# Kernel tuning notes

Hardware: AMD Instinct MI355X
Metric: run time of the kernel (lower is better)

Reference implementation:

```python
import jax, jax.numpy as jnp
import numpy as np

E4M3_MAX = 448.0
M, K, N = 131072, 512, 512


def _round_to_fp8_e4m3(x):
    # Emulated round-to-nearest E4M3: 3 mantissa bits, exponent in [-7, 8]
    abs_x = jnp.abs(x)
    sign = jnp.sign(x)
    exponent = jnp.clip(jnp.floor(jnp.log2(jnp.maximum(abs_x, 2.0 ** -9))), -7.0, 8.0)
    pow2e = jnp.exp2(exponent)
    mantissa = jnp.round(abs_x / pow2e * 8.0) / 8.0  # jnp.round is half-to-even, matching torch.round
    return sign * mantissa * pow2e


def _quantize_e4m3(x, scale):
    scaled = jnp.clip(x * scale, -E4M3_MAX, E4M3_MAX)
    return _round_to_fp8_e4m3(scaled)


def _dynamic_scale(x):
    # FP8TensorMeta.compute_scale with a single amax in history: max_value / amax * 0.9
    amax = jnp.max(jnp.abs(x))
    return jnp.where(amax > 0, E4M3_MAX / amax * 0.9, 1.0)


def setup_inputs() -> dict:
    key = jax.random.key(0)
    k1, k2, k3 = jax.random.split(key, 3)
    bound = 1.0 / np.sqrt(K)  # kaiming_uniform(a=sqrt(5)) on [N,K] -> U(-1/sqrt(K), 1/sqrt(K))
    x = jax.random.normal(k1, (M, K), dtype=jnp.float32)
    weight = jax.random.uniform(k2, (N, K), dtype=jnp.float32, minval=-bound, maxval=bound)
    bias = jax.random.uniform(k3, (N,), dtype=jnp.float32, minval=-bound, maxval=bound)
    return {"x": x, "weight": weight, "bias": bias}


def reference(x, weight, bias):
    input_scale = _dynamic_scale(x)
    weight_scale = _dynamic_scale(weight)
    x_fp8 = _quantize_e4m3(x, input_scale)          # [M, K]
    w_fp8 = _quantize_e4m3(weight, weight_scale)    # [N, K]
    out = jnp.einsum("mk,nk->mn", x_fp8, w_fp8) + bias  # F.linear
    return out / (input_scale * weight_scale)
```

## Files before the change

kernel.cpp:

```cpp
#include <hip/hip_runtime.h>

typedef unsigned short u16;
typedef unsigned int u32;
typedef unsigned char u8;
typedef __attribute__((ext_vector_type(4))) float f32x4;

template <bool HI>
__device__ __forceinline__ u32 q2fp8(float a, float b, u32 old, float s) {
  a = fminf(448.0f, fmaxf(-448.0f, a * s));
  b = fminf(448.0f, fmaxf(-448.0f, b * s));
  return (u32)__builtin_amdgcn_cvt_pk_fp8_f32(a, b, (int)old, HI);
}

__device__ __forceinline__ float block_max(float m) {
#pragma unroll
  for (int off = 32; off > 0; off >>= 1)
    m = fmaxf(m, __shfl_down(m, off, 64));
  __shared__ float sm[4];
  int wv = threadIdx.x >> 6;
  if ((threadIdx.x & 63) == 0) sm[wv] = m;
  __syncthreads();
  float r = fmaxf(fmaxf(sm[0], sm[1]), fmaxf(sm[2], sm[3]));
  __syncthreads();
  return r;
}

#define XBLOCKS 2048
#define WBLOCKS 64

__global__ void amax2_kernel(const float4* __restrict__ x, int nx4,
                             const float4* __restrict__ w, int nw4,
                             float* __restrict__ px, float* __restrict__ pw) {
  int bid = blockIdx.x;
  const float4* p;
  int n4, b, nb;
  float* dst;
  if (bid < XBLOCKS) { p = x; n4 = nx4; dst = px; b = bid; nb = XBLOCKS; }
  else { p = w; n4 = nw4; dst = pw; b = bid - XBLOCKS; nb = WBLOCKS; }
  float m = 0.0f;
  int stride = nb * 256;
  for (int i = b * 256 + threadIdx.x; i < n4; i += stride) {
    float4 v = p[i];
    m = fmaxf(m, fmaxf(fmaxf(fabsf(v.x), fabsf(v.y)), fmaxf(fabsf(v.z), fabsf(v.w))));
  }
  m = block_max(m);
  if (threadIdx.x == 0) dst[b] = m;
}

__global__ void scales_kernel(const float* __restrict__ px, const float* __restrict__ pw,
                              float* __restrict__ wsf) {
  int tid = threadIdx.x;
  float mx = 0.0f;
  for (int i = tid; i < XBLOCKS; i += 256) mx = fmaxf(mx, px[i]);
  mx = block_max(mx);
  float mw = tid < WBLOCKS ? pw[tid] : 0.0f;
  mw = block_max(mw);
  if (tid == 0) {
    float sx = mx > 0.0f ? 448.0f / mx * 0.9f : 1.0f;
    float sw = mw > 0.0f ? 448.0f / mw * 0.9f : 1.0f;
    wsf[2] = sx;
    wsf[3] = sw;
    wsf[4] = 1.0f / (sx * sw);
  }
}

__global__ void quant_w_kernel(const float* __restrict__ w, u8* __restrict__ wq,
                               const float* __restrict__ wsf) {
  const float sw = wsf[3];
  const int id = blockIdx.x * blockDim.x + threadIdx.x;
  const int kc = id >> 9;
  const int n = id & 511;
  const float4* src = (const float4*)(w + (size_t)n * 512 + kc * 8);
  const float4 a = src[0];
  const float4 b = src[1];
  uint2 r;
  r.x = q2fp8<false>(a.x, a.y, 0u, sw);
  r.x = q2fp8<true>(a.z, a.w, r.x, sw);
  r.y = q2fp8<false>(b.x, b.y, 0u, sw);
  r.y = q2fp8<true>(b.z, b.w, r.y, sw);
  *(uint2*)&wq[(size_t)kc * 4096 + n * 8] = r;
}

__global__ void __launch_bounds__(512, 4) gemm_kernel(const float* __restrict__ x,
                                                      const u8* __restrict__ wq,
                                                      const float* __restrict__ bias,
                                                      float* __restrict__ out,
                                                      const float* __restrict__ wsf) {
  __shared__ __align__(16) u8 As[2 * 8192];
  __shared__ __align__(16) u8 Bs[3 * 16384];
  const int tid = threadIdx.x;
  const int lane = tid & 63;
  const int wv = tid >> 6;
  const int quad = lane >> 4;
  const int lr = lane & 15;

  const int lin = blockIdx.x;
  const int xcd = lin & 7;
  const int jn = (lin >> 3) & 1;
  const int grp = lin >> 4;
  const int m0 = (grp * 8 + xcd) * 128;
  const int n0 = jn * 256;

  const float sx = wsf[2];
  const float inv = wsf[4];
  const int wm = (wv >> 2) * 64;
  const int wn = (wv & 3) * 64;
  const int xrow = tid >> 2;
  const int xq0 = (tid & 3) * 2;

  f32x4 acc[4][4] = {};
  float4 xr[4];

  auto stageB = [&](int bu, int kt) {
#pragma unroll
    for (int i = 0; i < 2; ++i) {
      const u8* gp = wq + (size_t)(kt * 8 + wv) * 4096 + (size_t)n0 * 8 + i * 1024 + lane * 16;
      u8* lp = &Bs[bu * 16384 + wv * 2048 + i * 1024 + lane * 16];
      __builtin_amdgcn_global_load_lds((const __attribute__((address_space(1))) u32*)gp,
                                       (__attribute__((address_space(3))) u32*)lp, 16, 0, 0);
    }
  };
  auto loadX = [&](int kt) {
    const float* p = x + (size_t)(m0 + xrow) * 512 + kt * 64 + xq0 * 8;
#pragma unroll
    for (int s = 0; s < 4; ++s) xr[s] = *(const float4*)(p + s * 4);
  };
  auto writeA = [&](int bu) {
#pragma unroll
    for (int j = 0; j < 2; ++j) {
      uint2 pk;
      pk.x = q2fp8<false>(xr[2 * j].x, xr[2 * j].y, 0u, sx);
      pk.x = q2fp8<true>(xr[2 * j].z, xr[2 * j].w, pk.x, sx);
      pk.y = q2fp8<false>(xr[2 * j + 1].x, xr[2 * j + 1].y, 0u, sx);
      pk.y = q2fp8<true>(xr[2 * j + 1].z, xr[2 * j + 1].w, pk.y, sx);
      *(uint2*)&As[bu * 8192 + (xq0 + j) * 1024 + xrow * 8] = pk;
    }
  };

  loadX(0);
  stageB(0, 0);
  stageB(1, 1);
  writeA(0);
  asm volatile("s_waitcnt vmcnt(2) lgkmcnt(0)" ::: "memory");
  __builtin_amdgcn_s_barrier();
  asm volatile("" ::: "memory");

#pragma unroll
  for (int kt = 0; kt < 8; ++kt) {
    const int cur3 = kt % 3;
    const int curA = kt & 1;
    if (kt < 7) loadX(kt + 1);
    if (kt < 6) stageB((kt + 2) % 3, kt + 2);
#pragma unroll
    for (int kk = 0; kk < 2; ++kk) {
      long af[4], bf[4];
#pragma unroll
      for (int mi = 0; mi < 4; ++mi)
        af[mi] = *(const long*)&As[curA * 8192 + (kk * 4 + quad) * 1024 + (wm + mi * 16 + lr) * 8];
#pragma unroll
      for (int ni = 0; ni < 4; ++ni)
        bf[ni] = *(const long*)&Bs[cur3 * 16384 + (kk * 4 + quad) * 2048 + (wn + ni * 16 + lr) * 8];
#pragma unroll
      for (int mi = 0; mi < 4; ++mi)
#pragma unroll
        for (int ni = 0; ni < 4; ++ni)
          acc[mi][ni] = __builtin_amdgcn_mfma_f32_16x16x32_fp8_fp8(af[mi], bf[ni], acc[mi][ni], 0, 0, 0);
    }
    if (kt < 7) writeA(curA ^ 1);
    asm volatile("s_waitcnt lgkmcnt(0)" ::: "memory");
    __builtin_amdgcn_s_barrier();
    asm volatile("" ::: "memory");
  }

  float bn[4];
#pragma unroll
  for (int ni = 0; ni < 4; ++ni) bn[ni] = bias[n0 + wn + ni * 16 + lr];
#pragma unroll
  for (int mi = 0; mi < 4; ++mi) {
    const int gr = m0 + wm + mi * 16 + quad * 4;
#pragma unroll
    for (int ni = 0; ni < 4; ++ni) {
      const int gc = n0 + wn + ni * 16 + lr;
#pragma unroll
      for (int j = 0; j < 4; ++j)
        out[(size_t)(gr + j) * 512 + gc] = (acc[mi][ni][j] + bn[ni]) * inv;
    }
  }
}

extern "C" void kernel_launch(void* const* d_in, const int* in_sizes, int n_in,
                              void* d_out, int out_size, void* d_ws, size_t ws_size,
                              hipStream_t stream) {
  const float* x = (const float*)d_in[0];
  const float* w = (const float*)d_in[1];
  const float* bias = (const float*)d_in[2];
  float* out = (float*)d_out;

  const int K = 512, N = 512;
  const int M = in_sizes[0] / K;

  float* ws_f = (float*)d_ws;
  float* px = ws_f + 16;
  float* pw = ws_f + 16 + XBLOCKS;
  u8* wq = (u8*)((char*)d_ws + 16384);

  hipLaunchKernelGGL(amax2_kernel, dim3(XBLOCKS + WBLOCKS), dim3(256), 0, stream,
                     (const float4*)x, (M * K) / 4, (const float4*)w, (N * K) / 4, px, pw);
  hipLaunchKernelGGL(scales_kernel, dim3(1), dim3(256), 0, stream, px, pw, ws_f);
  hipLaunchKernelGGL(quant_w_kernel, dim3((N * K / 8) / 256), dim3(256), 0, stream,
                     w, wq, ws_f);
  hipLaunchKernelGGL(gemm_kernel, dim3((M / 128) * 2), dim3(512), 0, stream,
                     x, wq, bias, out, ws_f);
}
```

Before: 519.1 us.

## Fold scale computation into consumers and deepen X prefetch to two stages

Removes the single-block scales kernel: quant_w and the GEMM now each reduce the per-block amax partials themselves and compute the scales locally. The GEMM prefetches X two k-tiles ahead using double register slots, switches the A tile in LDS to 16-byte rows with uint4 writes, and uses a partial vmcnt wait so loads stay in flight across the barrier. It also raises wave priority around the MFMA block. This saves one kernel launch and hides more global-load latency, at the cost of extra registers and redundant amax reductions in every block.

```diff
diff --git a/kernel.cpp b/kernel.cpp
--- a/kernel.cpp
+++ b/kernel.cpp
@@ -47,26 +47,16 @@
   if (threadIdx.x == 0) dst[b] = m;
 }
 
-__global__ void scales_kernel(const float* __restrict__ px, const float* __restrict__ pw,
-                              float* __restrict__ wsf) {
-  int tid = threadIdx.x;
-  float mx = 0.0f;
-  for (int i = tid; i < XBLOCKS; i += 256) mx = fmaxf(mx, px[i]);
-  mx = block_max(mx);
-  float mw = tid < WBLOCKS ? pw[tid] : 0.0f;
-  mw = block_max(mw);
-  if (tid == 0) {
-    float sx = mx > 0.0f ? 448.0f / mx * 0.9f : 1.0f;
-    float sw = mw > 0.0f ? 448.0f / mw * 0.9f : 1.0f;
-    wsf[2] = sx;
-    wsf[3] = sw;
-    wsf[4] = 1.0f / (sx * sw);
-  }
+__device__ __forceinline__ float wave_max64(float m) {
+#pragma unroll
+  for (int off = 32; off > 0; off >>= 1) m = fmaxf(m, __shfl_xor(m, off, 64));
+  return m;
 }
 
 __global__ void quant_w_kernel(const float* __restrict__ w, u8* __restrict__ wq,
-                               const float* __restrict__ wsf) {
-  const float sw = wsf[3];
+                               const float* __restrict__ pw) {
+  float mw = wave_max64(pw[threadIdx.x & 63]);
+  const float sw = mw > 0.0f ? 448.0f / mw * 0.9f : 1.0f;
   const int id = blockIdx.x * blockDim.x + threadIdx.x;
   const int kc = id >> 9;
   const int n = id & 511;
@@ -85,9 +75,11 @@
                                                       const u8* __restrict__ wq,
                                                       const float* __restrict__ bias,
                                                       float* __restrict__ out,
-                                                      const float* __restrict__ wsf) {
+                                                      const float* __restrict__ px,
+                                                      const float* __restrict__ pw) {
   __shared__ __align__(16) u8 As[2 * 8192];
   __shared__ __align__(16) u8 Bs[3 * 16384];
+  __shared__ float sm8[8];
   const int tid = threadIdx.x;
   const int lane = tid & 63;
   const int wv = tid >> 6;
@@ -101,15 +93,18 @@
   const int m0 = (grp * 8 + xcd) * 128;
   const int n0 = jn * 256;
 
-  const float sx = wsf[2];
-  const float inv = wsf[4];
   const int wm = (wv >> 2) * 64;
   const int wn = (wv & 3) * 64;
   const int xrow = tid >> 2;
-  const int xq0 = (tid & 3) * 2;
+  const int xc = tid & 3;
 
   f32x4 acc[4][4] = {};
-  float4 xr[4];
+  float4 xr[2][4];
+
+  float pxv[4];
+#pragma unroll
+  for (int i = 0; i < 4; ++i) pxv[i] = px[tid + i * 512];
+  float pwv = pw[lane];
 
   auto stageB = [&](int bu, int kt) {
 #pragma unroll
@@ -120,27 +115,43 @@
                                        (__attribute__((address_space(3))) u32*)lp, 16, 0, 0);
     }
   };
-  auto loadX = [&](int kt) {
-    const float* p = x + (size_t)(m0 + xrow) * 512 + kt * 64 + xq0 * 8;
-#pragma unroll
-    for (int s = 0; s < 4; ++s) xr[s] = *(const float4*)(p + s * 4);
+  auto loadX = [&](int slot, int kt) {
+    const float* p = x + (size_t)(m0 + xrow) * 512 + kt * 64 + xc * 16;
+#pragma unroll
+    for (int s = 0; s < 4; ++s) xr[slot][s] = *(const float4*)(p + s * 4);
   };
-  auto writeA = [&](int bu) {
-#pragma unroll
-    for (int j = 0; j < 2; ++j) {
-      uint2 pk;
-      pk.x = q2fp8<false>(xr[2 * j].x, xr[2 * j].y, 0u, sx);
-      pk.x = q2fp8<true>(xr[2 * j].z, xr[2 * j].w, pk.x, sx);
-      pk.y = q2fp8<false>(xr[2 * j + 1].x, xr[2 * j + 1].y, 0u, sx);
-      pk.y = q2fp8<true>(xr[2 * j + 1].z, xr[2 * j + 1].w, pk.y, sx);
-      *(uint2*)&As[bu * 8192 + (xq0 + j) * 1024 + xrow * 8] = pk;
-    }
-  };
-
-  loadX(0);
+
+  loadX(0, 0);
+  loadX(1, 1);
   stageB(0, 0);
   stageB(1, 1);
-  writeA(0);
+
+  float m = fmaxf(fmaxf(pxv[0], pxv[1]), fmaxf(pxv[2], pxv[3]));
+  m = wave_max64(m);
+  if (lane == 0) sm8[wv] = m;
+  __syncthreads();
+  float mx = sm8[0];
+#pragma unroll
+  for (int i = 1; i < 8; ++i) mx = fmaxf(mx, sm8[i]);
+  float mw = wave_max64(pwv);
+  const float sx = mx > 0.0f ? 448.0f / mx * 0.9f : 1.0f;
+  const float sw = mw > 0.0f ? 448.0f / mw * 0.9f : 1.0f;
+  const float inv = 1.0f / (sx * sw);
+
+  auto writeA = [&](int bu, int slot) {
+    uint4 pk;
+    pk.x = q2fp8<false>(xr[slot][0].x, xr[slot][0].y, 0u, sx);
+    pk.x = q2fp8<true>(xr[slot][0].z, xr[slot][0].w, pk.x, sx);
+    pk.y = q2fp8<false>(xr[slot][1].x, xr[slot][1].y, 0u, sx);
+    pk.y = q2fp8<true>(xr[slot][1].z, xr[slot][1].w, pk.y, sx);
+    pk.z = q2fp8<false>(xr[slot][2].x, xr[slot][2].y, 0u, sx);
+    pk.z = q2fp8<true>(xr[slot][2].z, xr[slot][2].w, pk.z, sx);
+    pk.w = q2fp8<false>(xr[slot][3].x, xr[slot][3].y, 0u, sx);
+    pk.w = q2fp8<true>(xr[slot][3].z, xr[slot][3].w, pk.w, sx);
+    *(uint4*)&As[bu * 8192 + xc * 2048 + xrow * 16] = pk;
+  };
+
+  writeA(0, 0);
   asm volatile("s_waitcnt vmcnt(2) lgkmcnt(0)" ::: "memory");
   __builtin_amdgcn_s_barrier();
   asm volatile("" ::: "memory");
@@ -149,27 +160,38 @@
   for (int kt = 0; kt < 8; ++kt) {
     const int cur3 = kt % 3;
     const int curA = kt & 1;
-    if (kt < 7) loadX(kt + 1);
-    if (kt < 6) stageB((kt + 2) % 3, kt + 2);
+    if (kt < 6) {
+      loadX(kt & 1, kt + 2);
+      stageB((kt + 2) % 3, kt + 2);
+    }
 #pragma unroll
     for (int kk = 0; kk < 2; ++kk) {
       long af[4], bf[4];
 #pragma unroll
       for (int mi = 0; mi < 4; ++mi)
-        af[mi] = *(const long*)&As[curA * 8192 + (kk * 4 + quad) * 1024 + (wm + mi * 16 + lr) * 8];
+        af[mi] = *(const long*)&As[curA * 8192 + (kk * 2 + (quad >> 1)) * 2048 +
+                                   (wm + mi * 16 + lr) * 16 + (quad & 1) * 8];
 #pragma unroll
       for (int ni = 0; ni < 4; ++ni)
         bf[ni] = *(const long*)&Bs[cur3 * 16384 + (kk * 4 + quad) * 2048 + (wn + ni * 16 + lr) * 8];
+      __builtin_amdgcn_s_setprio(1);
 #pragma unroll
       for (int mi = 0; mi < 4; ++mi)
 #pragma unroll
         for (int ni = 0; ni < 4; ++ni)
           acc[mi][ni] = __builtin_amdgcn_mfma_f32_16x16x32_fp8_fp8(af[mi], bf[ni], acc[mi][ni], 0, 0, 0);
-    }
-    if (kt < 7) writeA(curA ^ 1);
-    asm volatile("s_waitcnt lgkmcnt(0)" ::: "memory");
-    __builtin_amdgcn_s_barrier();
-    asm volatile("" ::: "memory");
+      __builtin_amdgcn_s_setprio(0);
+    }
+    if (kt < 7) {
+      writeA(curA ^ 1, (kt + 1) & 1);
+      if (kt < 6) {
+        asm volatile("s_waitcnt vmcnt(6) lgkmcnt(0)" ::: "memory");
+      } else {
+        asm volatile("s_waitcnt vmcnt(0) lgkmcnt(0)" ::: "memory");
+      }
+      __builtin_amdgcn_s_barrier();
+      asm volatile("" ::: "memory");
+    }
   }
 
   float bn[4];
@@ -206,9 +228,8 @@
 
   hipLaunchKernelGGL(amax2_kernel, dim3(XBLOCKS + WBLOCKS), dim3(256), 0, stream,
                      (const float4*)x, (M * K) / 4, (const float4*)w, (N * K) / 4, px, pw);
-  hipLaunchKernelGGL(scales_kernel, dim3(1), dim3(256), 0, stream, px, pw, ws_f);
   hipLaunchKernelGGL(quant_w_kernel, dim3((N * K / 8) / 256), dim3(256), 0, stream,
-                     w, wq, ws_f);
+                     w, wq, pw);
   hipLaunchKernelGGL(gemm_kernel, dim3((M / 128) * 2), dim3(512), 0, stream,
-                     x, wq, bias, out, ws_f);
-}
+                     x, wq, bias, out, px, pw);
+}
```

New measurement: 561.6 us. 1.08x slower.
